# Kernel optimization log

Measured on AMD Instinct MI355X. Metric: run time of the kernel, lower is better.

The kernel has to match this reference:

```python
import jax, jax.numpy as jnp
import numpy as np

N = 100000
E = 3200000
IN_C, HID_C, OUT_C = 128, 128, 64


def setup_inputs() -> dict:
    key = jax.random.key(0)
    k_x, k_e, k_w1, k_w2 = jax.random.split(key, 4)
    x = jax.random.normal(k_x, (N, IN_C), dtype=jnp.float32)
    edge_index = jax.random.randint(k_e, (2, E), 0, N, dtype=jnp.int64)
    # GCNConv uses Glorot-init weight [in, out] and zero bias
    W1 = jax.random.normal(k_w1, (IN_C, HID_C), dtype=jnp.float32) * (1.0 / np.sqrt(IN_C))
    b1 = jnp.zeros((HID_C,), dtype=jnp.float32)
    W2 = jax.random.normal(k_w2, (HID_C, OUT_C), dtype=jnp.float32) * (1.0 / np.sqrt(HID_C))
    b2 = jnp.zeros((OUT_C,), dtype=jnp.float32)
    return {"x": x, "edge_index": edge_index, "W1": W1, "b1": b1, "W2": W2, "b2": b2}


def _gcn_norm(edge_index, n_nodes):
    """Add self-loops and compute symmetric normalization coefficients."""
    loop = jnp.arange(n_nodes, dtype=edge_index.dtype)
    src = jnp.concatenate([edge_index[0], loop])  # [E+N]
    dst = jnp.concatenate([edge_index[1], loop])  # [E+N]
    ones = jnp.ones(src.shape[0], dtype=jnp.float32)
    deg = jax.ops.segment_sum(ones, dst, num_segments=n_nodes)  # in-degree w/ self loops
    dinv = jnp.where(deg > 0, jax.lax.rsqrt(deg), 0.0)
    norm = dinv[src] * dinv[dst]  # [E+N]
    return src, dst, norm


def _gcn_conv(x, W, b, src, dst, norm, n_nodes):
    h = x @ W                                   # [N, out] dense transform first (PyG order)
    msg = norm[:, None] * h[src]                # gather + scale  [E+N, out]
    out = jax.ops.segment_sum(msg, dst, num_segments=n_nodes)  # scatter-add
    return out + b


def reference(x, edge_index, W1, b1, W2, b2):
    src, dst, norm = _gcn_norm(edge_index, N)
    h = _gcn_conv(x, W1, b1, src, dst, norm, N)
    h = jax.nn.relu(h)
    out = _gcn_conv(h, W2, b2, src, dst, norm, N)
    return out
```

## Files before the change

### kernel.cpp

```cpp
#include <hip/hip_runtime.h>

typedef unsigned int u32;
typedef unsigned short u16;
typedef unsigned long long u64;
typedef __bf16 bf16x8 __attribute__((ext_vector_type(8)));
typedef float floatx4 __attribute__((ext_vector_type(4)));
typedef u32 u32x2 __attribute__((ext_vector_type(2)));
typedef u32 u32x4 __attribute__((ext_vector_type(4)));
typedef float floatx2 __attribute__((ext_vector_type(2)));

__device__ __forceinline__ u16 f2bf(float f) {
  u32 u = __float_as_uint(f);
  u += 0x7fffu + ((u >> 16) & 1u);
  return (u16)(u >> 16);
}
__device__ __forceinline__ float bf2f(u16 h) { return __uint_as_float(((u32)h) << 16); }
__device__ __forceinline__ float bflo(u32 v) { return __uint_as_float(v << 16); }
__device__ __forceinline__ float bfhi(u32 v) { return __uint_as_float(v & 0xffff0000u); }

#define SLICE_SH 10
#define SL (1 << SLICE_SH)
#define MAXNS 128

__global__ void probe_dtypes(const u16* __restrict__ xs, const u32* __restrict__ eis,
                             int* __restrict__ flags, int* __restrict__ scnt,
                             int* __restrict__ scur) {
  int lane = threadIdx.x;
  if (lane < MAXNS) { scnt[lane] = 0; scur[lane] = 0; }
  if (lane >= 64) return;
  int big = 0;
  for (int i = lane; i < 4096; i += 64) {
    u32 e = (xs[i] >> 7) & 0xffu;
    big += (e >= 0xC0u) ? 1 : 0;
  }
  int odd = 0;
  for (int i = lane; i < 256; i += 64)
    odd += (eis[2 * i + 1] != 0u) ? 1 : 0;
#pragma unroll
  for (int off = 32; off; off >>= 1) {
    big += __shfl_down(big, off);
    odd += __shfl_down(odd, off);
  }
  if (lane == 0 && blockIdx.x == 0) {
    flags[0] = (big > 16) ? 1 : 0;
    flags[1] = (odd == 0) ? 1 : 0;
  }
}


__global__ __launch_bounds__(256) void hist_pass(const int* __restrict__ ei,
                                                 const int* __restrict__ flags,
                                                 int* __restrict__ scnt, int e, int ns) {
  __shared__ int hist[MAXNS];
  int per = (e + gridDim.x - 1) / gridDim.x;
  int e0 = blockIdx.x * per;
  int e1 = e0 + per; if (e1 > e) e1 = e;
  for (int t = threadIdx.x; t < ns; t += 256) hist[t] = 0;
  __syncthreads();
  const int i64f = flags[1];
  for (int i = e0 + threadIdx.x; i < e1; i += 256) {
    int d = i64f ? ei[2 * (e + i)] : ei[e + i];
    atomicAdd(&hist[d >> SLICE_SH], 1);
  }
  __syncthreads();
  for (int t = threadIdx.x; t < ns; t += 256)
    atomicAdd(&scnt[t], hist[t]);
}

__global__ __launch_bounds__(256) void bin_pass(const int* __restrict__ ei,
                                                const int* __restrict__ flags,
                                                const int* __restrict__ scnt,
                                                int* __restrict__ scur,
                                                u64* __restrict__ staged,
                                                int e, int ns) {
  __shared__ int hist[MAXNS];
  __shared__ int curs[MAXNS];
  __shared__ int sb[MAXNS];
  int per = (e + gridDim.x - 1) / gridDim.x;
  int e0 = blockIdx.x * per;
  int e1 = e0 + per; if (e1 > e) e1 = e;
  const int i64f = flags[1];
  for (int t = threadIdx.x; t < ns; t += 256) hist[t] = 0;
  if (threadIdx.x < MAXNS) sb[threadIdx.x] = (threadIdx.x < ns) ? scnt[threadIdx.x] : 0;
  __syncthreads();
  for (int i = e0 + threadIdx.x; i < e1; i += 256) {
    int d = i64f ? ei[2 * (e + i)] : ei[e + i];
    atomicAdd(&hist[d >> SLICE_SH], 1);
  }
  __syncthreads();
  for (int off = 1; off < MAXNS; off <<= 1) {
    int v = 0;
    if (threadIdx.x < MAXNS && threadIdx.x >= off) v = sb[threadIdx.x - off];
    __syncthreads();
    if (threadIdx.x < MAXNS) sb[threadIdx.x] += v;
    __syncthreads();
  }
  for (int t = threadIdx.x; t < ns; t += 256)
    curs[t] = (t ? sb[t - 1] : 0) + atomicAdd(&scur[t], hist[t]);
  __syncthreads();
  int i = e0 + threadIdx.x;
  for (; i + 768 < e1; i += 1024) {
    int d[4], s[4], pos[4];
#pragma unroll
    for (int p = 0; p < 4; p++) {
      int ii = i + 256 * p;
      if (i64f) { s[p] = ei[2 * ii]; d[p] = ei[2 * (e + ii)]; }
      else      { s[p] = ei[ii];     d[p] = ei[e + ii]; }
    }
#pragma unroll
    for (int p = 0; p < 4; p++) pos[p] = atomicAdd(&curs[d[p] >> SLICE_SH], 1);
#pragma unroll
    for (int p = 0; p < 4; p++)
      staged[pos[p]] = ((u64)(u32)d[p] << 32) | (u32)s[p];
  }
  for (; i < e1; i += 256) {
    int s, d;
    if (i64f) { s = ei[2 * i]; d = ei[2 * (e + i)]; }
    else      { s = ei[i];     d = ei[e + i]; }
    staged[atomicAdd(&curs[d >> SLICE_SH], 1)] = ((u64)(u32)d << 32) | (u32)s;
  }
}

__global__ __launch_bounds__(1024) void fill_slice2(const u64* __restrict__ staged,
                                                    const int* __restrict__ scnt,
                                                    int* __restrict__ rp,
                                                    float* __restrict__ dinv,
                                                    int* __restrict__ csr, int n, int ns) {
  __shared__ int cnt[SL];
  __shared__ int part[SL];
  __shared__ int sb[MAXNS];
  const int s = blockIdx.x;
  const int base = s << SLICE_SH;
  const int tid = threadIdx.x;
  cnt[tid] = 0;
  if (tid < MAXNS) sb[tid] = (tid < ns) ? scnt[tid] : 0;
  __syncthreads();
  for (int off = 1; off < MAXNS; off <<= 1) {
    int v = 0;
    if (tid < MAXNS && tid >= off) v = sb[tid - off];
    __syncthreads();
    if (tid < MAXNS) sb[tid] += v;
    __syncthreads();
  }
  const int lo = s ? sb[s - 1] : 0;
  const int hi = sb[s];
  if (s == ns - 1 && tid == 0) rp[n] = hi;
  {
    int i = lo + tid;
    for (; i + 7168 < hi; i += 8192) {
      int b[8];
#pragma unroll
      for (int p = 0; p < 8; p++) b[p] = (int)(staged[i + 1024 * p] >> 32) & (SL - 1);
#pragma unroll
      for (int p = 0; p < 8; p++) atomicAdd(&cnt[b[p]], 1);
    }
    for (; i < hi; i += 1024)
      atomicAdd(&cnt[(int)(staged[i] >> 32) & (SL - 1)], 1);
  }
  __syncthreads();
  int c0 = cnt[tid];
  part[tid] = c0;
  __syncthreads();
  for (int off = 1; off < SL; off <<= 1) {
    int t = (tid >= off) ? part[tid - off] : 0;
    __syncthreads();
    part[tid] += t;
    __syncthreads();
  }
  int p0 = lo + (tid ? part[tid - 1] : 0);
  __syncthreads();
  cnt[tid] = p0;
  int d0 = base + tid;
  if (d0 < n) { rp[d0] = p0; dinv[d0] = rsqrtf((float)(c0 + 1)); }
  __syncthreads();
  {
    int i = lo + tid;
    for (; i + 7168 < hi; i += 8192) {
      u64 pr[8]; int pos[8];
#pragma unroll
      for (int p = 0; p < 8; p++) pr[p] = staged[i + 1024 * p];
#pragma unroll
      for (int p = 0; p < 8; p++)
        pos[p] = atomicAdd(&cnt[(int)(pr[p] >> 32) & (SL - 1)], 1);
#pragma unroll
      for (int p = 0; p < 8; p++) csr[pos[p]] = (int)(pr[p] & 0xffffffffu);
    }
    for (; i < hi; i += 1024) {
      u64 pr = staged[i];
      int pos = atomicAdd(&cnt[(int)(pr >> 32) & (SL - 1)], 1);
      csr[pos] = (int)(pr & 0xffffffffu);
    }
  }
}


template <int OUT, bool XPROBED>
__global__ __launch_bounds__(256) void gemm_x_w(const void* __restrict__ Xv,
                                                const void* __restrict__ Wv,
                                                const int* __restrict__ flags,
                                                u16* __restrict__ Y, int nrows) {
  constexpr int K = 128;
  constexpr int NT = OUT / 16;
  constexpr int LDW = K + 8;
  __shared__ u16 Wt[OUT * LDW];
  const int wf32 = flags[0];
  const int xf32 = XPROBED ? wf32 : 0;
  int tid = threadIdx.x;
  if (wf32) {
    const float* Wf = (const float*)Wv;
    for (int idx = tid; idx < K * OUT; idx += 256) {
      int k = idx / OUT, n = idx % OUT;
      Wt[n * LDW + k] = f2bf(Wf[idx]);
    }
  } else {
    const u16* Wu = (const u16*)Wv;
    for (int idx = tid; idx < K * OUT; idx += 256) {
      int k = idx / OUT, n = idx % OUT;
      Wt[n * LDW + k] = Wu[idx];
    }
  }
  __syncthreads();
  int lane = tid & 63, wave = tid >> 6;
  int quad = lane >> 4, low = lane & 15;
  int mBase = blockIdx.x * 64 + wave * 16;
  int m = mBase + low;
  int ml = (m < nrows) ? m : (nrows - 1);
  floatx4 acc[NT];
#pragma unroll
  for (int i = 0; i < NT; i++) acc[i] = (floatx4)0.0f;
#pragma unroll
  for (int kb = 0; kb < 4; kb++) {
    int k0 = kb * 32 + quad * 8;
    bf16x8 a;
    if (xf32) {
      const float* Xf = (const float*)Xv;
      floatx4 p0 = *(const floatx4*)(Xf + (size_t)ml * K + k0);
      floatx4 p1 = *(const floatx4*)(Xf + (size_t)ml * K + k0 + 4);
      union { bf16x8 v; u16 s[8]; } au;
#pragma unroll
      for (int j = 0; j < 4; j++) { au.s[j] = f2bf(p0[j]); au.s[4 + j] = f2bf(p1[j]); }
      a = au.v;
    } else {
      a = *(const bf16x8*)((const u16*)Xv + (size_t)ml * K + k0);
    }
#pragma unroll
    for (int nt = 0; nt < NT; nt++) {
      bf16x8 b = *(const bf16x8*)(&Wt[(nt * 16 + low) * LDW + k0]);
      acc[nt] = __builtin_amdgcn_mfma_f32_16x16x32_bf16(a, b, acc[nt], 0, 0, 0);
    }
  }
#pragma unroll
  for (int nt = 0; nt < NT; nt++) {
    int col = nt * 16 + low;
#pragma unroll
    for (int r = 0; r < 4; r++) {
      int row = mBase + quad * 4 + r;
      if (row < nrows) Y[(size_t)row * OUT + col] = f2bf(acc[nt][r]);
    }
  }
}


__global__ __launch_bounds__(256) void agg_128(const u32* __restrict__ H,
                                               const int* __restrict__ rp,
                                               const int* __restrict__ cs,
                                               const float* __restrict__ dinv,
                                               const void* __restrict__ biasv,
                                               const int* __restrict__ flags,
                                               u32* __restrict__ out, int n) {
  int node = blockIdx.x * 4 + (threadIdx.x >> 6);
  if (node >= n) return;
  int lane = threadIdx.x & 63;
  int e4 = lane >> 4, c = lane & 15;
  int s0 = rp[node], s1 = rp[node + 1];
  float a[8] = {0.f, 0.f, 0.f, 0.f, 0.f, 0.f, 0.f, 0.f};
  for (int base = s0; base < s1; base += 64) {
    int nb = s1 - base; if (nb > 64) nb = 64;
    int src = 0; float dv = 0.f;
    if (lane < nb) { src = cs[base + lane]; dv = dinv[src]; }
    for (int j = 0; j < nb; j += 16) {
      u32x4 v[4]; float w[4];
#pragma unroll
      for (int p = 0; p < 4; p++) {
        int idx = j + 4 * p + e4;
        int sj = __shfl(src, idx);
        w[p] = __shfl(dv, idx);
        v[p] = *(const u32x4*)(H + (size_t)sj * 64 + 4 * c);
      }
#pragma unroll
      for (int p = 0; p < 4; p++) {
#pragma unroll
        for (int k = 0; k < 4; k++) {
          a[2 * k]     += w[p] * bflo(v[p][k]);
          a[2 * k + 1] += w[p] * bfhi(v[p][k]);
        }
      }
    }
  }
#pragma unroll
  for (int k = 0; k < 8; k++) {
    a[k] += __shfl_xor(a[k], 16);
    a[k] += __shfl_xor(a[k], 32);
  }
  float ds = dinv[node];
  u32x4 vs = *(const u32x4*)(H + (size_t)node * 64 + 4 * c);
  float r[8];
#pragma unroll
  for (int k = 0; k < 4; k++) {
    r[2 * k]     = ds * (a[2 * k]     + ds * bflo(vs[k]));
    r[2 * k + 1] = ds * (a[2 * k + 1] + ds * bfhi(vs[k]));
  }
  if (flags[0]) {
    floatx4 b0 = *(const floatx4*)((const float*)biasv + 8 * c);
    floatx4 b1 = *(const floatx4*)((const float*)biasv + 8 * c + 4);
#pragma unroll
    for (int k = 0; k < 4; k++) { r[k] += b0[k]; r[4 + k] += b1[k]; }
  } else {
    u32x4 bb = *(const u32x4*)((const u32*)biasv + 4 * c);
#pragma unroll
    for (int k = 0; k < 4; k++) { r[2 * k] += bflo(bb[k]); r[2 * k + 1] += bfhi(bb[k]); }
  }
#pragma unroll
  for (int k = 0; k < 8; k++) r[k] = fmaxf(r[k], 0.f);
  if (e4 == 0) {
    u32x4 o;
#pragma unroll
    for (int k = 0; k < 4; k++)
      o[k] = (u32)f2bf(r[2 * k]) | ((u32)f2bf(r[2 * k + 1]) << 16);
    *(u32x4*)(out + (size_t)node * 64 + 4 * c) = o;
  }
}

__global__ __launch_bounds__(256) void agg_64(const u16* __restrict__ Hu,
                                              const int* __restrict__ rp,
                                              const int* __restrict__ cs,
                                              const float* __restrict__ dinv,
                                              const void* __restrict__ biasv,
                                              const int* __restrict__ flags,
                                              void* __restrict__ outv, int n) {
  const u32* H = (const u32*)Hu;
  int node = blockIdx.x * 4 + (threadIdx.x >> 6);
  if (node >= n) return;
  int lane = threadIdx.x & 63;
  int e4 = lane >> 4, c = lane & 15;
  int s0 = rp[node], s1 = rp[node + 1];
  float a[4] = {0.f, 0.f, 0.f, 0.f};
  for (int base = s0; base < s1; base += 64) {
    int nb = s1 - base; if (nb > 64) nb = 64;
    int src = 0; float dv = 0.f;
    if (lane < nb) { src = cs[base + lane]; dv = dinv[src]; }
    for (int j = 0; j < nb; j += 16) {
      u32x2 v[4]; float w[4];
#pragma unroll
      for (int p = 0; p < 4; p++) {
        int idx = j + 4 * p + e4;
        int sj = __shfl(src, idx);
        w[p] = __shfl(dv, idx);
        v[p] = *(const u32x2*)(H + (size_t)sj * 32 + 2 * c);
      }
#pragma unroll
      for (int p = 0; p < 4; p++) {
        a[0] += w[p] * bflo(v[p].x); a[1] += w[p] * bfhi(v[p].x);
        a[2] += w[p] * bflo(v[p].y); a[3] += w[p] * bfhi(v[p].y);
      }
    }
  }
#pragma unroll
  for (int k = 0; k < 4; k++) {
    a[k] += __shfl_xor(a[k], 16);
    a[k] += __shfl_xor(a[k], 32);
  }
  float ds = dinv[node];
  u32x2 vs = *(const u32x2*)(H + (size_t)node * 32 + 2 * c);
  float r0 = ds * (a[0] + ds * bflo(vs.x));
  float r1 = ds * (a[1] + ds * bfhi(vs.x));
  float r2 = ds * (a[2] + ds * bflo(vs.y));
  float r3 = ds * (a[3] + ds * bfhi(vs.y));
  if (flags[0]) {
    floatx4 bf = *(const floatx4*)((const float*)biasv + 4 * c);
    r0 += bf[0]; r1 += bf[1]; r2 += bf[2]; r3 += bf[3];
    if (e4 == 0) {
      floatx4 o; o[0] = r0; o[1] = r1; o[2] = r2; o[3] = r3;
      *(floatx4*)((float*)outv + (size_t)node * 64 + 4 * c) = o;
    }
  } else {
    u32x2 bb = *(const u32x2*)((const u32*)biasv + 2 * c);
    r0 += bflo(bb.x); r1 += bfhi(bb.x); r2 += bflo(bb.y); r3 += bfhi(bb.y);
    if (e4 == 0) {
      u32x2 o;
      o.x = (u32)f2bf(r0) | ((u32)f2bf(r1) << 16);
      o.y = (u32)f2bf(r2) | ((u32)f2bf(r3) << 16);
      *(u32x2*)((u32*)outv + (size_t)node * 32 + 2 * c) = o;
    }
  }
}


extern "C" void kernel_launch(void* const* d_in, const int* in_sizes, int n_in,
                              void* d_out, int out_size, void* d_ws, size_t ws_size,
                              hipStream_t stream) {
  const void* x  = d_in[0];
  const int*  ei = (const int*)d_in[1];
  const void* W1 = d_in[2];
  const void* b1 = d_in[3];
  const void* W2 = d_in[4];
  const void* b2 = d_in[5];
  const int N = in_sizes[0] / 128;
  const int E = in_sizes[1] / 2;
  const int NS = (N + SL - 1) >> SLICE_SH;

  auto al = [](size_t v) { return (v + 255) & ~(size_t)255; };
  char* ws = (char*)d_ws;
  size_t o = 0;
  int*   flags = (int*)(ws + o);  o += 256;
  int*   scnt  = (int*)(ws + o);  o += 512;
  int*   scur  = (int*)(ws + o);  o += 512;
  int*   rp    = (int*)(ws + o);  o += al((size_t)(N + 1) * 4);
  float* dinv  = (float*)(ws + o); o += al((size_t)N * 4);
  int*   csr   = (int*)(ws + o);  o += al((size_t)E * 4);
  u16*   h     = (u16*)(ws + o);  o += al((size_t)N * 128 * 2);
  u16*   h1    = (u16*)(ws + o);  o += al((size_t)N * 128 * 2);
  u16*   h2    = h;
  u64* staged = (u64*)h;

  probe_dtypes<<<1, 128, 0, stream>>>((const u16*)x, (const u32*)ei, flags, scnt, scur);
  hist_pass<<<1280, 256, 0, stream>>>(ei, flags, scnt, E, NS);
  bin_pass<<<1280, 256, 0, stream>>>(ei, flags, scnt, scur, staged, E, NS);
  fill_slice2<<<NS, 1024, 0, stream>>>(staged, scnt, rp, dinv, csr, N, NS);

  gemm_x_w<128, true><<<(N + 63) / 64, 256, 0, stream>>>(x, W1, flags, h, N);
  agg_128<<<(N + 3) / 4, 256, 0, stream>>>((const u32*)h, rp, csr, dinv, b1, flags, (u32*)h1, N);
  gemm_x_w<64, false><<<(N + 63) / 64, 256, 0, stream>>>(h1, W2, flags, h2, N);
  agg_64<<<(N + 3) / 4, 256, 0, stream>>>(h2, rp, csr, dinv, b2, flags, d_out, N);
}
```

Baseline: 425.3 us.

## Drop global slice histogram pass and fuse edge binning with first GEMM

```diff
diff --git a/kernel.cpp b/kernel.cpp
--- a/kernel.cpp
+++ b/kernel.cpp
@@ -14,19 +14,18 @@
   u += 0x7fffu + ((u >> 16) & 1u);
   return (u16)(u >> 16);
 }
-__device__ __forceinline__ float bf2f(u16 h) { return __uint_as_float(((u32)h) << 16); }
 __device__ __forceinline__ float bflo(u32 v) { return __uint_as_float(v << 16); }
 __device__ __forceinline__ float bfhi(u32 v) { return __uint_as_float(v & 0xffff0000u); }
 
 #define SLICE_SH 10
 #define SL (1 << SLICE_SH)
 #define MAXNS 128
+#define NBBIN 1280
 
 __global__ void probe_dtypes(const u16* __restrict__ xs, const u32* __restrict__ eis,
-                             int* __restrict__ flags, int* __restrict__ scnt,
-                             int* __restrict__ scur) {
+                             int* __restrict__ flags, int* __restrict__ scur) {
   int lane = threadIdx.x;
-  if (lane < MAXNS) { scnt[lane] = 0; scur[lane] = 0; }
+  if (lane < MAXNS) scur[lane] = 0;
   if (lane >= 64) return;
   int big = 0;
   for (int i = lane; i < 4096; i += 64) {
@@ -48,161 +47,15 @@
 }
 
 
-__global__ __launch_bounds__(256) void hist_pass(const int* __restrict__ ei,
-                                                 const int* __restrict__ flags,
-                                                 int* __restrict__ scnt, int e, int ns) {
-  __shared__ int hist[MAXNS];
-  int per = (e + gridDim.x - 1) / gridDim.x;
-  int e0 = blockIdx.x * per;
-  int e1 = e0 + per; if (e1 > e) e1 = e;
-  for (int t = threadIdx.x; t < ns; t += 256) hist[t] = 0;
-  __syncthreads();
-  const int i64f = flags[1];
-  for (int i = e0 + threadIdx.x; i < e1; i += 256) {
-    int d = i64f ? ei[2 * (e + i)] : ei[e + i];
-    atomicAdd(&hist[d >> SLICE_SH], 1);
-  }
-  __syncthreads();
-  for (int t = threadIdx.x; t < ns; t += 256)
-    atomicAdd(&scnt[t], hist[t]);
-}
-
-__global__ __launch_bounds__(256) void bin_pass(const int* __restrict__ ei,
-                                                const int* __restrict__ flags,
-                                                const int* __restrict__ scnt,
-                                                int* __restrict__ scur,
-                                                u64* __restrict__ staged,
-                                                int e, int ns) {
-  __shared__ int hist[MAXNS];
-  __shared__ int curs[MAXNS];
-  __shared__ int sb[MAXNS];
-  int per = (e + gridDim.x - 1) / gridDim.x;
-  int e0 = blockIdx.x * per;
-  int e1 = e0 + per; if (e1 > e) e1 = e;
-  const int i64f = flags[1];
-  for (int t = threadIdx.x; t < ns; t += 256) hist[t] = 0;
-  if (threadIdx.x < MAXNS) sb[threadIdx.x] = (threadIdx.x < ns) ? scnt[threadIdx.x] : 0;
-  __syncthreads();
-  for (int i = e0 + threadIdx.x; i < e1; i += 256) {
-    int d = i64f ? ei[2 * (e + i)] : ei[e + i];
-    atomicAdd(&hist[d >> SLICE_SH], 1);
-  }
-  __syncthreads();
-  for (int off = 1; off < MAXNS; off <<= 1) {
-    int v = 0;
-    if (threadIdx.x < MAXNS && threadIdx.x >= off) v = sb[threadIdx.x - off];
-    __syncthreads();
-    if (threadIdx.x < MAXNS) sb[threadIdx.x] += v;
-    __syncthreads();
-  }
-  for (int t = threadIdx.x; t < ns; t += 256)
-    curs[t] = (t ? sb[t - 1] : 0) + atomicAdd(&scur[t], hist[t]);
-  __syncthreads();
-  int i = e0 + threadIdx.x;
-  for (; i + 768 < e1; i += 1024) {
-    int d[4], s[4], pos[4];
-#pragma unroll
-    for (int p = 0; p < 4; p++) {
-      int ii = i + 256 * p;
-      if (i64f) { s[p] = ei[2 * ii]; d[p] = ei[2 * (e + ii)]; }
-      else      { s[p] = ei[ii];     d[p] = ei[e + ii]; }
-    }
-#pragma unroll
-    for (int p = 0; p < 4; p++) pos[p] = atomicAdd(&curs[d[p] >> SLICE_SH], 1);
-#pragma unroll
-    for (int p = 0; p < 4; p++)
-      staged[pos[p]] = ((u64)(u32)d[p] << 32) | (u32)s[p];
-  }
-  for (; i < e1; i += 256) {
-    int s, d;
-    if (i64f) { s = ei[2 * i]; d = ei[2 * (e + i)]; }
-    else      { s = ei[i];     d = ei[e + i]; }
-    staged[atomicAdd(&curs[d >> SLICE_SH], 1)] = ((u64)(u32)d << 32) | (u32)s;
-  }
-}
-
-__global__ __launch_bounds__(1024) void fill_slice2(const u64* __restrict__ staged,
-                                                    const int* __restrict__ scnt,
-                                                    int* __restrict__ rp,
-                                                    float* __restrict__ dinv,
-                                                    int* __restrict__ csr, int n, int ns) {
-  __shared__ int cnt[SL];
-  __shared__ int part[SL];
-  __shared__ int sb[MAXNS];
-  const int s = blockIdx.x;
-  const int base = s << SLICE_SH;
-  const int tid = threadIdx.x;
-  cnt[tid] = 0;
-  if (tid < MAXNS) sb[tid] = (tid < ns) ? scnt[tid] : 0;
-  __syncthreads();
-  for (int off = 1; off < MAXNS; off <<= 1) {
-    int v = 0;
-    if (tid < MAXNS && tid >= off) v = sb[tid - off];
-    __syncthreads();
-    if (tid < MAXNS) sb[tid] += v;
-    __syncthreads();
-  }
-  const int lo = s ? sb[s - 1] : 0;
-  const int hi = sb[s];
-  if (s == ns - 1 && tid == 0) rp[n] = hi;
-  {
-    int i = lo + tid;
-    for (; i + 7168 < hi; i += 8192) {
-      int b[8];
-#pragma unroll
-      for (int p = 0; p < 8; p++) b[p] = (int)(staged[i + 1024 * p] >> 32) & (SL - 1);
-#pragma unroll
-      for (int p = 0; p < 8; p++) atomicAdd(&cnt[b[p]], 1);
-    }
-    for (; i < hi; i += 1024)
-      atomicAdd(&cnt[(int)(staged[i] >> 32) & (SL - 1)], 1);
-  }
-  __syncthreads();
-  int c0 = cnt[tid];
-  part[tid] = c0;
-  __syncthreads();
-  for (int off = 1; off < SL; off <<= 1) {
-    int t = (tid >= off) ? part[tid - off] : 0;
-    __syncthreads();
-    part[tid] += t;
-    __syncthreads();
-  }
-  int p0 = lo + (tid ? part[tid - 1] : 0);
-  __syncthreads();
-  cnt[tid] = p0;
-  int d0 = base + tid;
-  if (d0 < n) { rp[d0] = p0; dinv[d0] = rsqrtf((float)(c0 + 1)); }
-  __syncthreads();
-  {
-    int i = lo + tid;
-    for (; i + 7168 < hi; i += 8192) {
-      u64 pr[8]; int pos[8];
-#pragma unroll
-      for (int p = 0; p < 8; p++) pr[p] = staged[i + 1024 * p];
-#pragma unroll
-      for (int p = 0; p < 8; p++)
-        pos[p] = atomicAdd(&cnt[(int)(pr[p] >> 32) & (SL - 1)], 1);
-#pragma unroll
-      for (int p = 0; p < 8; p++) csr[pos[p]] = (int)(pr[p] & 0xffffffffu);
-    }
-    for (; i < hi; i += 1024) {
-      u64 pr = staged[i];
-      int pos = atomicAdd(&cnt[(int)(pr >> 32) & (SL - 1)], 1);
-      csr[pos] = (int)(pr & 0xffffffffu);
-    }
-  }
-}
-
-
 template <int OUT, bool XPROBED>
-__global__ __launch_bounds__(256) void gemm_x_w(const void* __restrict__ Xv,
-                                                const void* __restrict__ Wv,
-                                                const int* __restrict__ flags,
-                                                u16* __restrict__ Y, int nrows) {
+__device__ __forceinline__ void gemm_body(const void* __restrict__ Xv,
+                                          const void* __restrict__ Wv,
+                                          const int* __restrict__ flags,
+                                          u16* __restrict__ Y, int nrows,
+                                          int bid, u16* Wt) {
   constexpr int K = 128;
   constexpr int NT = OUT / 16;
   constexpr int LDW = K + 8;
-  __shared__ u16 Wt[OUT * LDW];
   const int wf32 = flags[0];
   const int xf32 = XPROBED ? wf32 : 0;
   int tid = threadIdx.x;
@@ -222,7 +75,7 @@
   __syncthreads();
   int lane = tid & 63, wave = tid >> 6;
   int quad = lane >> 4, low = lane & 15;
-  int mBase = blockIdx.x * 64 + wave * 16;
+  int mBase = bid * 64 + wave * 16;
   int m = mBase + low;
   int ml = (m < nrows) ? m : (nrows - 1);
   floatx4 acc[NT];
@@ -256,6 +109,160 @@
     for (int r = 0; r < 4; r++) {
       int row = mBase + quad * 4 + r;
       if (row < nrows) Y[(size_t)row * OUT + col] = f2bf(acc[nt][r]);
+    }
+  }
+}
+
+__device__ __forceinline__ void bin_body(const int* __restrict__ ei,
+                                         const int* __restrict__ flags,
+                                         int* __restrict__ scur,
+                                         u64* __restrict__ stA, u64* __restrict__ stB,
+                                         int splitS, int cap, int e, int ns,
+                                         int bid, int* hist, int* curs) {
+  int per = (e + NBBIN - 1) / NBBIN;
+  int e0 = bid * per;
+  int e1 = e0 + per; if (e1 > e) e1 = e;
+  const int i64f = flags[1];
+  for (int t = threadIdx.x; t < ns; t += 256) hist[t] = 0;
+  __syncthreads();
+  for (int i = e0 + threadIdx.x; i < e1; i += 256) {
+    int d = i64f ? ei[2 * (e + i)] : ei[e + i];
+    atomicAdd(&hist[d >> SLICE_SH], 1);
+  }
+  __syncthreads();
+  for (int t = threadIdx.x; t < ns; t += 256)
+    curs[t] = atomicAdd(&scur[t], hist[t]);
+  __syncthreads();
+  int i = e0 + threadIdx.x;
+  for (; i + 768 < e1; i += 1024) {
+    int d[4], s[4], pos[4];
+#pragma unroll
+    for (int p = 0; p < 4; p++) {
+      int ii = i + 256 * p;
+      if (i64f) { s[p] = ei[2 * ii]; d[p] = ei[2 * (e + ii)]; }
+      else      { s[p] = ei[ii];     d[p] = ei[e + ii]; }
+    }
+#pragma unroll
+    for (int p = 0; p < 4; p++) pos[p] = atomicAdd(&curs[d[p] >> SLICE_SH], 1);
+#pragma unroll
+    for (int p = 0; p < 4; p++) {
+      int sl = d[p] >> SLICE_SH;
+      u64* st = (sl < splitS) ? stA + (size_t)sl * cap : stB + (size_t)(sl - splitS) * cap;
+      st[pos[p]] = ((u64)(u32)d[p] << 32) | (u32)s[p];
+    }
+  }
+  for (; i < e1; i += 256) {
+    int s, d;
+    if (i64f) { s = ei[2 * i]; d = ei[2 * (e + i)]; }
+    else      { s = ei[i];     d = ei[e + i]; }
+    int sl = d >> SLICE_SH;
+    u64* st = (sl < splitS) ? stA + (size_t)sl * cap : stB + (size_t)(sl - splitS) * cap;
+    st[atomicAdd(&curs[sl], 1)] = ((u64)(u32)d << 32) | (u32)s;
+  }
+}
+
+__global__ __launch_bounds__(256) void gemm1_bin(const void* __restrict__ Xv,
+                                                 const void* __restrict__ Wv,
+                                                 const int* __restrict__ flags,
+                                                 u16* __restrict__ Y, int nrows, int nbGemm,
+                                                 const int* __restrict__ ei,
+                                                 int* __restrict__ scur,
+                                                 u64* __restrict__ stA, u64* __restrict__ stB,
+                                                 int splitS, int cap, int e, int ns) {
+  __shared__ __attribute__((aligned(16))) char smbuf[128 * 136 * 2];
+  int id = blockIdx.x;
+  int small = (NBBIN < nbGemm) ? NBBIN : nbGemm;
+  int isBin, bid;
+  if (id < 2 * small) { isBin = !(id & 1); bid = id >> 1; }
+  else { bid = small + (id - 2 * small); isBin = (NBBIN > nbGemm); }
+  if (isBin) {
+    int* hist = (int*)smbuf;
+    int* curs = hist + MAXNS;
+    bin_body(ei, flags, scur, stA, stB, splitS, cap, e, ns, bid, hist, curs);
+  } else {
+    gemm_body<128, true>(Xv, Wv, flags, Y, nrows, bid, (u16*)smbuf);
+  }
+}
+
+__global__ __launch_bounds__(256) void gemm2_k(const void* __restrict__ Xv,
+                                               const void* __restrict__ Wv,
+                                               const int* __restrict__ flags,
+                                               u16* __restrict__ Y, int nrows) {
+  __shared__ u16 Wt[64 * 136];
+  gemm_body<64, false>(Xv, Wv, flags, Y, nrows, blockIdx.x, Wt);
+}
+
+__global__ __launch_bounds__(1024) void fill_slice3(const u64* __restrict__ stA,
+                                                    const u64* __restrict__ stB,
+                                                    const int* __restrict__ scur,
+                                                    int* __restrict__ rp,
+                                                    float* __restrict__ dinv,
+                                                    int* __restrict__ csr,
+                                                    int splitS, int cap, int n, int ns) {
+  __shared__ int cnt[SL];
+  __shared__ int part[SL];
+  __shared__ int sb[MAXNS];
+  const int s = blockIdx.x;
+  const int base = s << SLICE_SH;
+  const int tid = threadIdx.x;
+  cnt[tid] = 0;
+  if (tid < MAXNS) sb[tid] = (tid < ns) ? scur[tid] : 0;
+  __syncthreads();
+  for (int off = 1; off < MAXNS; off <<= 1) {
+    int v = 0;
+    if (tid < MAXNS && tid >= off) v = sb[tid - off];
+    __syncthreads();
+    if (tid < MAXNS) sb[tid] += v;
+    __syncthreads();
+  }
+  const int csrLo = s ? sb[s - 1] : 0;
+  const int m = sb[s] - csrLo;
+  if (s == ns - 1 && tid == 0) rp[n] = sb[ns - 1];
+  const u64* st = (s < splitS) ? stA + (size_t)s * cap : stB + (size_t)(s - splitS) * cap;
+  {
+    int i = tid;
+    for (; i + 7168 < m; i += 8192) {
+      int b[8];
+#pragma unroll
+      for (int p = 0; p < 8; p++) b[p] = (int)(st[i + 1024 * p] >> 32) & (SL - 1);
+#pragma unroll
+      for (int p = 0; p < 8; p++) atomicAdd(&cnt[b[p]], 1);
+    }
+    for (; i < m; i += 1024)
+      atomicAdd(&cnt[(int)(st[i] >> 32) & (SL - 1)], 1);
+  }
+  __syncthreads();
+  int c0 = cnt[tid];
+  part[tid] = c0;
+  __syncthreads();
+  for (int off = 1; off < SL; off <<= 1) {
+    int t = (tid >= off) ? part[tid - off] : 0;
+    __syncthreads();
+    part[tid] += t;
+    __syncthreads();
+  }
+  int p0 = csrLo + (tid ? part[tid - 1] : 0);
+  __syncthreads();
+  cnt[tid] = p0;
+  int d0 = base + tid;
+  if (d0 < n) { rp[d0] = p0; dinv[d0] = rsqrtf((float)(c0 + 1)); }
+  __syncthreads();
+  {
+    int i = tid;
+    for (; i + 7168 < m; i += 8192) {
+      u64 pr[8]; int pos[8];
+#pragma unroll
+      for (int p = 0; p < 8; p++) pr[p] = st[i + 1024 * p];
+#pragma unroll
+      for (int p = 0; p < 8; p++)
+        pos[p] = atomicAdd(&cnt[(int)(pr[p] >> 32) & (SL - 1)], 1);
+#pragma unroll
+      for (int p = 0; p < 8; p++) csr[pos[p]] = (int)(pr[p] & 0xffffffffu);
+    }
+    for (; i < m; i += 1024) {
+      u64 pr = st[i];
+      int pos = atomicAdd(&cnt[(int)(pr >> 32) & (SL - 1)], 1);
+      csr[pos] = (int)(pr & 0xffffffffu);
     }
   }
 }
@@ -409,11 +416,16 @@
   const int E = in_sizes[1] / 2;
   const int NS = (N + SL - 1) >> SLICE_SH;
 
+  int CAP = (E + NS - 1) / NS;
+  CAP += CAP / 8;
+  size_t doutSlots = ((size_t)out_size * 2) / 8;
+  int SPLIT = (int)(doutSlots / (size_t)CAP);
+  if (SPLIT > NS) SPLIT = NS;
+
   auto al = [](size_t v) { return (v + 255) & ~(size_t)255; };
   char* ws = (char*)d_ws;
   size_t o = 0;
   int*   flags = (int*)(ws + o);  o += 256;
-  int*   scnt  = (int*)(ws + o);  o += 512;
   int*   scur  = (int*)(ws + o);  o += 512;
   int*   rp    = (int*)(ws + o);  o += al((size_t)(N + 1) * 4);
   float* dinv  = (float*)(ws + o); o += al((size_t)N * 4);
@@ -421,15 +433,16 @@
   u16*   h     = (u16*)(ws + o);  o += al((size_t)N * 128 * 2);
   u16*   h1    = (u16*)(ws + o);  o += al((size_t)N * 128 * 2);
   u16*   h2    = h;
-  u64* staged = (u64*)h;
-
-  probe_dtypes<<<1, 128, 0, stream>>>((const u16*)x, (const u32*)ei, flags, scnt, scur);
-  hist_pass<<<1280, 256, 0, stream>>>(ei, flags, scnt, E, NS);
-  bin_pass<<<1280, 256, 0, stream>>>(ei, flags, scnt, scur, staged, E, NS);
-  fill_slice2<<<NS, 1024, 0, stream>>>(staged, scnt, rp, dinv, csr, N, NS);
-
-  gemm_x_w<128, true><<<(N + 63) / 64, 256, 0, stream>>>(x, W1, flags, h, N);
+  u64* stA = (u64*)d_out;
+  u64* stB = (u64*)h1;
+
+  const int nbGemm = (N + 63) / 64;
+
+  probe_dtypes<<<1, 128, 0, stream>>>((const u16*)x, (const u32*)ei, flags, scur);
+  gemm1_bin<<<NBBIN + nbGemm, 256, 0, stream>>>(x, W1, flags, h, N, nbGemm,
+                                                ei, scur, stA, stB, SPLIT, CAP, E, NS);
+  fill_slice3<<<NS, 1024, 0, stream>>>(stA, stB, scur, rp, dinv, csr, SPLIT, CAP, N, NS);
   agg_128<<<(N + 3) / 4, 256, 0, stream>>>((const u32*)h, rp, csr, dinv, b1, flags, (u32*)h1, N);
-  gemm_x_w<64, false><<<(N + 63) / 64, 256, 0, stream>>>(h1, W2, flags, h2, N);
+  gemm2_k<<<nbGemm, 256, 0, stream>>>(h1, W2, flags, h2, N);
   agg_64<<<(N + 3) / 4, 256, 0, stream>>>(h2, rp, csr, dinv, b2, flags, d_out, N);
 }
```

Result: faster. 384.2 us (-9.7%).
